# Kernel tuning notes

Hardware: AMD Instinct MI355X
Metric: run time of the kernel (lower is better)

## Reference

```python
import jax, jax.numpy as jnp
import numpy as np

B, T, E = 64, 2048, 256  # batch, max seq len, embedding_dim; hidden_dim = 1

def setup_inputs() -> dict:
    key = jax.random.key(0)
    k1, k2, k3, k4, k5, k6 = jax.random.split(key, 6)
    data = jax.random.normal(k1, (B, T, E), dtype=jnp.float32)
    seq_length = jax.random.randint(k2, (B,), 1, T + 1)
    seq_length = seq_length.at[0].set(T)  # ensure padded output length == T (static)
    s = 1.0  # uniform(-1,1) init in torch; use scaled normal params
    w_ih = (jax.random.normal(k3, (4, E), dtype=jnp.float32) * 0.05)
    w_hh = (jax.random.normal(k4, (4, 1), dtype=jnp.float32) * 0.05)
    b_ih = (jax.random.normal(k5, (4,), dtype=jnp.float32) * 0.05)
    b_hh = (jax.random.normal(k6, (4,), dtype=jnp.float32) * 0.05)
    return {"data": data, "seq_length": seq_length,
            "w_ih": w_ih, "w_hh": w_hh, "b_ih": b_ih, "b_hh": b_hh}

def _lstm_scan(data, w_ih, w_hh, b_ih, b_hh):
    b, t, e = data.shape
    # precompute input projections for all timesteps: [B, T, 4] (gate order i,f,g,o)
    xg = jnp.einsum('bte,ge->btg', data, w_ih) + b_ih + b_hh
    w_hh_row = w_hh[:, 0]  # [4], hidden_dim == 1

    def step(carry, x_t):
        h, c = carry                      # [B,1] each
        g = x_t + h * w_hh_row            # [B,4]
        i = jax.nn.sigmoid(g[:, 0:1])
        f = jax.nn.sigmoid(g[:, 1:2])
        gg = jnp.tanh(g[:, 2:3])
        o = jax.nn.sigmoid(g[:, 3:4])
        c = f * c + i * gg
        h = o * jnp.tanh(c)
        return (h, c), h

    h0 = jnp.zeros((b, 1), data.dtype)
    (_, _), hs = jax.lax.scan(step, (h0, h0), jnp.swapaxes(xg, 0, 1))  # [T,B,1]
    return jnp.swapaxes(hs, 0, 1)  # [B,T,1]

def reference(data, seq_length, w_ih, w_hh, b_ih, b_hh):
    hs = _lstm_scan(data, w_ih, w_hh, b_ih, b_hh)  # [B,T,1]
    # pad_packed_sequence zero-fills positions t >= len; sigmoid is applied AFTER,
    # so padded positions become sigmoid(0) = 0.5 (faithful to the torch module).
    t = data.shape[1]
    mask = (jnp.arange(t)[None, :] < seq_length[:, None])[..., None]
    out = jax.nn.sigmoid(jnp.where(mask, hs, jnp.zeros_like(hs)))
    return out, seq_length
```

## Files before the change

kernel.cpp:

```cpp
#include <hip/hip_runtime.h>


#define NLOG2E   (-1.4426950408889634f)
#define TWOLOG2E ( 2.8853900817779268f)

constexpr int Bb = 64;
constexpr int Tt = 2048;
constexpr int Ee = 256;

__global__ __launch_bounds__(256) void xg_kernel(
    const float* __restrict__ data, const float* __restrict__ w_ih,
    const float* __restrict__ b_ih, const float* __restrict__ b_hh,
    float* __restrict__ xg)
{
    const int g   = threadIdx.x & 3;
    const int row = blockIdx.x * 64 + (threadIdx.x >> 2);
    const float4* dp = (const float4*)data + (size_t)row * (Ee / 4);
    const float4* wp = (const float4*)(w_ih + g * Ee);

    float ax = 0.f, ay = 0.f, az = 0.f, aw = 0.f;
    #pragma unroll 16
    for (int j = 0; j < Ee / 4; ++j) {
        const float4 d = dp[j];
        const float4 w = wp[j];
        ax = fmaf(d.x, w.x, ax);
        ay = fmaf(d.y, w.y, ay);
        az = fmaf(d.z, w.z, az);
        aw = fmaf(d.w, w.w, aw);
    }
    const float s     = (ax + ay) + (az + aw);
    const float bias  = b_ih[g] + b_hh[g];
    const float scale = (g == 2) ? TWOLOG2E : NLOG2E;
    const int b = row >> 11;
    const int t = row & (Tt - 1);
    xg[(t * Bb + b) * 4 + g] = scale * (s + bias);
}

__device__ __forceinline__ float sig_from_scaled(float a) {
    return __builtin_amdgcn_rcpf(1.0f + __builtin_amdgcn_exp2f(a));
}
__device__ __forceinline__ float tanh_from_scaled(float a) {
    return 1.0f - 2.0f * __builtin_amdgcn_rcpf(1.0f + __builtin_amdgcn_exp2f(a));
}

__global__ __launch_bounds__(64) void scan_kernel(
    const float* __restrict__ xg, const float* __restrict__ w_hh,
    const int* __restrict__ seq_length, float* __restrict__ out)
{
    const int b = threadIdx.x;
    const int chunk = blockIdx.x;
    const float wi = NLOG2E   * w_hh[0];
    const float wf = NLOG2E   * w_hh[1];
    const float wg = TWOLOG2E * w_hh[2];
    const float wo = NLOG2E   * w_hh[3];
    const int len = seq_length[b];

    const float4* x4   = (const float4*)xg;
    float4*       orow = (float4*)(out + (size_t)b * Tt);

    const int warmG = (chunk == 0) ? 0 : 8;
    const int g0    = chunk * 8 - warmG;
    const int nG    = warmG + 8;

    float h = 0.0f, c = 0.0f;

    float4 r0[4], r1[4], r2[4], r3[4];
    #pragma unroll
    for (int i = 0; i < 4; ++i) {
        r0[i] = x4[((g0 + 0) * 4 + i) * Bb + b];
        r1[i] = x4[((g0 + 1) * 4 + i) * Bb + b];
        r2[i] = x4[((g0 + 2) * 4 + i) * Bb + b];
        r3[i] = x4[((g0 + 3) * 4 + i) * Bb + b];
    }

#define STEP(xv)                                                   \
    {                                                              \
        const float ai = fmaf(h, wi, (xv).x);                      \
        const float af = fmaf(h, wf, (xv).y);                      \
        const float ag = fmaf(h, wg, (xv).z);                      \
        const float ao = fmaf(h, wo, (xv).w);                      \
        const float i_ = sig_from_scaled(ai);                      \
        const float f_ = sig_from_scaled(af);                      \
        const float g_ = tanh_from_scaled(ag);                     \
        const float o_ = sig_from_scaled(ao);                      \
        c = fmaf(f_, c, i_ * g_);                                  \
        h = o_ * tanh_from_scaled(TWOLOG2E * c);                   \
    }
#define OUTV(t_) sig_from_scaled(NLOG2E * (((t_) < len) ? h : 0.0f))

#define BODY(j, slot)                                              \
    {                                                              \
        const int gg = g0 + (j);                                   \
        const int tt = gg * 4;                                     \
        float4 ov;                                                 \
        STEP(slot[0]); ov.x = OUTV(tt + 0);                        \
        STEP(slot[1]); ov.y = OUTV(tt + 1);                        \
        STEP(slot[2]); ov.z = OUTV(tt + 2);                        \
        STEP(slot[3]); ov.w = OUTV(tt + 3);                        \
        if ((j) >= warmG) orow[gg] = ov;                           \
        if ((j) + 4 < nG) {                                        \
            const int tp = (gg + 4) * 4;                           \
            slot[0] = x4[(tp + 0) * Bb + b];                       \
            slot[1] = x4[(tp + 1) * Bb + b];                       \
            slot[2] = x4[(tp + 2) * Bb + b];                       \
            slot[3] = x4[(tp + 3) * Bb + b];                       \
        }                                                          \
    }

    const int nM = nG >> 2;
    for (int m = 0; m < nM; ++m) {
        const int j = m * 4;
        BODY(j + 0, r0);
        BODY(j + 1, r1);
        BODY(j + 2, r2);
        BODY(j + 3, r3);
    }
#undef BODY
#undef STEP
#undef OUTV

    if (chunk == 0) out[(size_t)Bb * Tt + b] = (float)len;
}

extern "C" void kernel_launch(void* const* d_in, const int* in_sizes, int n_in,
                              void* d_out, int out_size, void* d_ws, size_t ws_size,
                              hipStream_t stream) {
    const float* data = (const float*)d_in[0];
    const int*   seq  = (const int*)  d_in[1];
    const float* w_ih = (const float*)d_in[2];
    const float* w_hh = (const float*)d_in[3];
    const float* b_ih = (const float*)d_in[4];
    const float* b_hh = (const float*)d_in[5];
    float* out = (float*)d_out;
    float* xg  = (float*)d_ws;

    xg_kernel<<<dim3(Bb * Tt / 64), dim3(256), 0, stream>>>(data, w_ih, b_ih, b_hh, xg);
    scan_kernel<<<dim3(Tt / 32), dim3(64), 0, stream>>>(xg, w_hh, seq, out);
}
```

Measured before the change: 229.8 us.

## Stage data tiles into LDS via direct global-to-LDS loads in projection kernel

The input projection kernel now copies each 64-row tile of data into padded shared memory using global_load_lds. Two waves then each reduce half of the embedding dimension for all four gates per row, and a shared-memory reduction combines the halves before writing one float4 per row. The goal is coalesced full-row loads instead of each thread striding through its own row, and reuse of every loaded data element across the four gates. In exchange it uses about 68KB of LDS per 128-thread block, which may limit occupancy, and adds two barriers.

```diff
diff --git a/kernel.cpp b/kernel.cpp
--- a/kernel.cpp
+++ b/kernel.cpp
@@ -7,33 +7,71 @@
 constexpr int Bb = 64;
 constexpr int Tt = 2048;
 constexpr int Ee = 256;
+constexpr int TILE = 64;
+constexpr int STRW = 260;
 
-__global__ __launch_bounds__(256) void xg_kernel(
+__global__ __launch_bounds__(128) void xg_kernel(
     const float* __restrict__ data, const float* __restrict__ w_ih,
     const float* __restrict__ b_ih, const float* __restrict__ b_hh,
     float* __restrict__ xg)
 {
-    const int g   = threadIdx.x & 3;
-    const int row = blockIdx.x * 64 + (threadIdx.x >> 2);
-    const float4* dp = (const float4*)data + (size_t)row * (Ee / 4);
-    const float4* wp = (const float4*)(w_ih + g * Ee);
+    __shared__ float lds[TILE * STRW + 2 * TILE * 4];
+    float4* red4 = (float4*)&lds[TILE * STRW];
 
-    float ax = 0.f, ay = 0.f, az = 0.f, aw = 0.f;
-    #pragma unroll 16
-    for (int j = 0; j < Ee / 4; ++j) {
-        const float4 d = dp[j];
-        const float4 w = wp[j];
-        ax = fmaf(d.x, w.x, ax);
-        ay = fmaf(d.y, w.y, ay);
-        az = fmaf(d.z, w.z, az);
-        aw = fmaf(d.w, w.w, aw);
+    const int tid = threadIdx.x;
+    const int l   = tid & 63;
+    const int w   = __builtin_amdgcn_readfirstlane(tid >> 6);
+
+    const size_t tilebase = (size_t)blockIdx.x * TILE * Ee;
+    #pragma unroll
+    for (int i = 0; i < 32; ++i) {
+        const int r = w * 32 + i;
+        __builtin_amdgcn_global_load_lds(
+            (const __attribute__((address_space(1))) void*)(data + tilebase + (size_t)r * Ee + l * 4),
+            (__attribute__((address_space(3))) void*)&lds[r * STRW],
+            16, 0, 0);
     }
-    const float s     = (ax + ay) + (az + aw);
-    const float bias  = b_ih[g] + b_hh[g];
-    const float scale = (g == 2) ? TWOLOG2E : NLOG2E;
-    const int b = row >> 11;
-    const int t = row & (Tt - 1);
-    xg[(t * Bb + b) * 4 + g] = scale * (s + bias);
+    __syncthreads();
+
+    const float*  dr = &lds[l * STRW];
+    const float4* wl = (const float4*)w_ih;
+
+    float s0 = 0.f, s1 = 0.f, s2 = 0.f, s3 = 0.f;
+    #pragma unroll 4
+    for (int jj = 0; jj < 32; ++jj) {
+        const int j = w * 32 + jj;
+        const float4 d  = *(const float4*)(dr + 4 * j);
+        const float4 w0 = wl[       j];
+        const float4 w1 = wl[ 64 +  j];
+        const float4 w2 = wl[128 +  j];
+        const float4 w3 = wl[192 +  j];
+        s0 = fmaf(d.w, w0.w, fmaf(d.z, w0.z, fmaf(d.y, w0.y, fmaf(d.x, w0.x, s0))));
+        s1 = fmaf(d.w, w1.w, fmaf(d.z, w1.z, fmaf(d.y, w1.y, fmaf(d.x, w1.x, s1))));
+        s2 = fmaf(d.w, w2.w, fmaf(d.z, w2.z, fmaf(d.y, w2.y, fmaf(d.x, w2.x, s2))));
+        s3 = fmaf(d.w, w3.w, fmaf(d.z, w3.z, fmaf(d.y, w3.y, fmaf(d.x, w3.x, s3))));
+    }
+
+    float4 part; part.x = s0; part.y = s1; part.z = s2; part.w = s3;
+    red4[w * TILE + l] = part;
+    __syncthreads();
+
+    if (w == 0) {
+        const float4 a = red4[l];
+        const float4 b2 = red4[TILE + l];
+        const float g0 = a.x + b2.x + b_ih[0] + b_hh[0];
+        const float g1 = a.y + b2.y + b_ih[1] + b_hh[1];
+        const float g2 = a.z + b2.z + b_ih[2] + b_hh[2];
+        const float g3 = a.w + b2.w + b_ih[3] + b_hh[3];
+        float4 v;
+        v.x = NLOG2E   * g0;
+        v.y = NLOG2E   * g1;
+        v.z = TWOLOG2E * g2;
+        v.w = NLOG2E   * g3;
+        const int row = blockIdx.x * TILE + l;
+        const int b   = row >> 11;
+        const int tg  = row & (Tt - 1);
+        ((float4*)xg)[tg * Bb + b] = v;
+    }
 }
 
 __device__ __forceinline__ float sig_from_scaled(float a) {
@@ -134,6 +172,6 @@
     float* out = (float*)d_out;
     float* xg  = (float*)d_ws;
 
-    xg_kernel<<<dim3(Bb * Tt / 64), dim3(256), 0, stream>>>(data, w_ih, b_ih, b_hh, xg);
+    xg_kernel<<<dim3(Bb * Tt / TILE), dim3(128), 0, stream>>>(data, w_ih, b_ih, b_hh, xg);
     scan_kernel<<<dim3(Tt / 32), dim3(64), 0, stream>>>(xg, w_hh, seq, out);
 }
```

New measurement: 205.6 us. 10.5% less time.
